# Kernel tuning notes

Measured on AMD Instinct MI355X. Metric: run time of the kernel, lower is better.

Reference implementation:

```python
import jax, jax.numpy as jnp
import numpy as np

N_HEAD = 16
N_KV = 4
HEAD_DIM = 128
WINDOW = 1024
SINK = 4
THETA = 10000.0


def _rope_cos_sin(T, dim, theta, dtype):
    inv_freq = 1.0 / (theta ** (jnp.arange(0, dim, 2, dtype=jnp.float32) / dim))
    t = jnp.arange(T, dtype=jnp.float32)
    ang = jnp.outer(t, inv_freq)  # [T, dim/2]
    return jnp.cos(ang).astype(dtype), jnp.sin(ang).astype(dtype)


def _apply_rope(x, cos, sin):
    # x: [B, H, T, D]; cos/sin: [T, D/2]
    d2 = x.shape[-1] // 2
    x1, x2 = x[..., :d2], x[..., d2:]
    return jnp.concatenate([x1 * cos - x2 * sin, x2 * cos + x1 * sin], axis=-1)


def setup_inputs() -> dict:
    key = jax.random.key(0)
    ks = jax.random.split(key, 5)
    B, T, C = 2, 2048, 2048
    x = jax.random.normal(ks[0], (B, T, C), dtype=jnp.float32)
    s = 0.02
    wq = jax.random.normal(ks[1], (C, C), dtype=jnp.float32) * s
    wk = jax.random.normal(ks[2], (N_KV * HEAD_DIM, C), dtype=jnp.float32) * s
    wv = jax.random.normal(ks[3], (N_KV * HEAD_DIM, C), dtype=jnp.float32) * s
    wo = jax.random.normal(ks[4], (C, C), dtype=jnp.float32) * s
    return {"x": x, "wq": wq, "wk": wk, "wv": wv, "wo": wo}


def reference(x, wq, wk, wv, wo):
    B, T, C = x.shape
    # QKV projections (Linear with weight [out, in], no bias)
    q = (x @ wq.T).reshape(B, T, N_HEAD, HEAD_DIM).transpose(0, 2, 1, 3)  # [B,H,T,D]
    k = (x @ wk.T).reshape(B, T, N_KV, HEAD_DIM).transpose(0, 2, 1, 3)    # [B,Hkv,T,D]
    v = (x @ wv.T).reshape(B, T, N_KV, HEAD_DIM).transpose(0, 2, 1, 3)

    cos, sin = _rope_cos_sin(T, HEAD_DIM, THETA, x.dtype)
    q = _apply_rope(q, cos, sin)
    k = _apply_rope(k, cos, sin)

    # GQA: repeat kv heads to match query heads (repeat_interleave on head dim)
    rep = N_HEAD // N_KV
    k = jnp.repeat(k, rep, axis=1)
    v = jnp.repeat(v, rep, axis=1)

    # causal + sliding window + attention sink mask
    i = jnp.arange(T)[:, None]
    j = jnp.arange(T)[None, :]
    allowed = (j <= i) & (((i - j) <= WINDOW) | (j < SINK))
    bias = jnp.where(allowed, 0.0, -jnp.inf).astype(x.dtype)  # [T,T]

    scale = 1.0 / np.sqrt(HEAD_DIM)
    att = jnp.einsum("bhqd,bhkd->bhqk", q, k) * scale + bias
    att = jax.nn.softmax(att, axis=-1)
    y = jnp.einsum("bhqk,bhkd->bhqd", att, v)  # [B,H,T,D]
    y = y.transpose(0, 2, 1, 3).reshape(B, T, C)
    return y @ wo.T
```

## Files before the change

kernel.cpp:

```cpp
#include <hip/hip_runtime.h>
#include <hip/hip_bf16.h>

typedef __bf16 bf16x8 __attribute__((ext_vector_type(8)));
typedef __bf16 bf16x4 __attribute__((ext_vector_type(4)));
typedef float  f32x4  __attribute__((ext_vector_type(4)));
typedef unsigned int uint4v __attribute__((ext_vector_type(4)));

#define NB     2
#define TT     2048
#define CC     2048
#define NH     16
#define NKV    4
#define HD     128
#define WIN    1024
#define SINKN  4
#define QSCALE 0.08838834764831845f

__device__ __forceinline__ void lds_load16(const void* g, void* l) {
    __builtin_amdgcn_global_load_lds(
        (__attribute__((address_space(1))) void*)const_cast<void*>(g),
        (__attribute__((address_space(3))) void*)l, 16, 0, 0);
}

__device__ __forceinline__ unsigned pack2bf(float a, float b) {
    __bf16 x = (__bf16)a, y = (__bf16)b;
    unsigned short ux = __builtin_bit_cast(unsigned short, x);
    unsigned short uy = __builtin_bit_cast(unsigned short, y);
    return (unsigned)ux | ((unsigned)uy << 16);
}

__global__ void cvt_kernel(const float* __restrict__ in, __bf16* __restrict__ out, int n) {
    int idx = (blockIdx.x * blockDim.x + threadIdx.x) * 4;
    const int stride = gridDim.x * blockDim.x * 4;
    for (; idx < n; idx += stride) {
        const float4 v = *(const float4*)(in + idx);
        bf16x4 o;
        o[0] = (__bf16)v.x; o[1] = (__bf16)v.y; o[2] = (__bf16)v.z; o[3] = (__bf16)v.w;
        *(bf16x4*)(out + idx) = o;
    }
}

__global__ void cvt_w_kernel(const float* __restrict__ wq, const float* __restrict__ wk,
                             const float* __restrict__ wv, const float* __restrict__ wo,
                             __bf16* __restrict__ out) {
    int idx = (blockIdx.x * blockDim.x + threadIdx.x) * 4;
    const int stride = gridDim.x * blockDim.x * 4;
    for (; idx < 10485760; idx += stride) {
        const float* src; int off;
        if (idx < 4194304)      { src = wq; off = idx; }
        else if (idx < 5242880) { src = wk; off = idx - 4194304; }
        else if (idx < 6291456) { src = wv; off = idx - 5242880; }
        else                    { src = wo; off = idx - 6291456; }
        const float4 v = *(const float4*)(src + off);
        bf16x4 o;
        o[0] = (__bf16)v.x; o[1] = (__bf16)v.y; o[2] = (__bf16)v.z; o[3] = (__bf16)v.w;
        *(bf16x4*)(out + idx) = o;
    }
}

__global__ void rope_table_kernel(float* __restrict__ cosT, float* __restrict__ sinT) {
    const int i = blockIdx.x * blockDim.x + threadIdx.x;
    const int t = i >> 6, d = i & 63;
    const float inv_freq = 1.0f / powf(10000.0f, (float)d * (1.0f / 64.0f));
    const float ang = (float)t * inv_freq;
    cosT[i] = cosf(ang);
    sinT[i] = sinf(ang);
}

__global__ void rope_scatter_kernel(const __bf16* __restrict__ qkv,
                                    const float* __restrict__ cosT,
                                    const float* __restrict__ sinT,
                                    __bf16* __restrict__ Qo,
                                    __bf16* __restrict__ Ko) {
    const int job = blockIdx.x * 256 + threadIdx.x;
    int m, d8, base_off; __bf16* outp; float scale;
    if (job < 524288) {
        m = job >> 7;
        const int pj = job & 127;
        const int hh = pj >> 3; d8 = pj & 7;
        base_off = hh * 128;
        const int b = m >> 11, t = m & 2047;
        outp = Qo + ((size_t)(b * NH + hh) * TT + t) * HD + d8 * 8;
        scale = QSCALE;
    } else {
        const int j2 = job - 524288;
        m = j2 >> 5;
        const int pj = j2 & 31;
        const int g = pj >> 3; d8 = pj & 7;
        base_off = 2048 + g * 128;
        const int b = m >> 11, t = m & 2047;
        outp = Ko + ((size_t)(b * NKV + g) * TT + t) * HD + d8 * 8;
        scale = 1.0f;
    }
    const int t = m & 2047;
    const __bf16* row = qkv + (size_t)m * 3072 + base_off + d8 * 8;
    const bf16x8 x1 = *(const bf16x8*)row;
    const bf16x8 x2 = *(const bf16x8*)(row + 64);
    const float4 c0 = *(const float4*)(cosT + t * 64 + d8 * 8);
    const float4 c1 = *(const float4*)(cosT + t * 64 + d8 * 8 + 4);
    const float4 s0 = *(const float4*)(sinT + t * 64 + d8 * 8);
    const float4 s1 = *(const float4*)(sinT + t * 64 + d8 * 8 + 4);
    const float cs[8] = {c0.x, c0.y, c0.z, c0.w, c1.x, c1.y, c1.z, c1.w};
    const float sn[8] = {s0.x, s0.y, s0.z, s0.w, s1.x, s1.y, s1.z, s1.w};
    bf16x8 o1, o2;
#pragma unroll
    for (int e = 0; e < 8; ++e) {
        const float a = (float)x1[e], bb = (float)x2[e];
        o1[e] = (__bf16)((a * cs[e] - bb * sn[e]) * scale);
        o2[e] = (__bf16)((bb * cs[e] + a * sn[e]) * scale);
    }
    *(bf16x8*)outp = o1;
    *(bf16x8*)(outp + 64) = o2;
}

__global__ void v_transpose_kernel(const __bf16* __restrict__ qkv, __bf16* __restrict__ Vt) {
    __shared__ __bf16 tile[64][72];
    const int bkv = blockIdx.z;
    const int b = bkv >> 2, g = bkv & 3;
    const int t0 = blockIdx.x << 6, d0 = blockIdx.y << 6;
    const int r = threadIdx.x >> 2, cg = threadIdx.x & 3;
    const __bf16* src = qkv + (size_t)(b * TT + t0 + r) * 3072 + 2560 + g * 128 + d0 + cg * 16;
    *(bf16x8*)&tile[r][cg * 16]     = *(const bf16x8*)src;
    *(bf16x8*)&tile[r][cg * 16 + 8] = *(const bf16x8*)(src + 8);
    __syncthreads();
    __bf16* dst = Vt + ((size_t)bkv * HD + d0 + r) * TT + t0 + cg * 16;
    bf16x8 o0, o1;
#pragma unroll
    for (int c2 = 0; c2 < 8; ++c2) {
        o0[c2] = tile[cg * 16 + c2][r];
        o1[c2] = tile[cg * 16 + 8 + c2][r];
    }
    *(bf16x8*)dst = o0;
    *(bf16x8*)(dst + 8) = o1;
}

template <int OUT_BF16>
__global__ __launch_bounds__(512, 2) void gemm_bt8(const __bf16* __restrict__ A,
                                                   const __bf16* __restrict__ Bm,
                                                   void* __restrict__ C,
                                                   int M, int N, int K) {
    __shared__ __align__(16) __bf16 lA[2][256 * 64];
    __shared__ __align__(16) __bf16 lB[2][256 * 64];
    const int tid = threadIdx.x;
    const int lane = tid & 63;
    const int w = tid >> 6;
    const int wm = w >> 2, wn = w & 3;
    const int nbn = N >> 8;
    const int bm = blockIdx.x / nbn, bn = blockIdx.x % nbn;
    const int m0 = bm << 8, n0 = bn << 8;
    const int lr = lane & 15, lh = lane >> 4;
    const int NT = K >> 6;

    auto stageA = [&](int kt, int buf, int i) {
        const int d = i * 8192 + tid * 16;
        const int row = d >> 7;
        const int colb = (d & 127) ^ ((row & 7) << 4);
        lds_load16(A + (size_t)(m0 + row) * K + kt * 64 + (colb >> 1),
                   (char*)lA[buf] + i * 8192 + w * 1024);
    };
    auto stageB = [&](int kt, int buf, int i) {
        const int d = i * 8192 + tid * 16;
        const int row = d >> 7;
        const int colb = (d & 127) ^ ((row & 7) << 4);
        lds_load16(Bm + (size_t)(n0 + row) * K + kt * 64 + (colb >> 1),
                   (char*)lB[buf] + i * 8192 + w * 1024);
    };

    f32x4 acc[8][4] = {};

#pragma unroll
    for (int i = 0; i < 4; ++i) stageA(0, 0, i);
#pragma unroll
    for (int i = 0; i < 4; ++i) stageB(0, 0, i);
    asm volatile("s_waitcnt vmcnt(0)" ::: "memory");
    __syncthreads();

    for (int kt = 0; kt < NT; ++kt) {
        const int cur = kt & 1, nxt = cur ^ 1;
        const bool pf = (kt + 1 < NT);
        const char* bA = (const char*)lA[cur];
        const char* bB = (const char*)lB[cur];

        bf16x8 aF[4][2], b0[2][2], b1[2][2];
#pragma unroll
        for (int mf = 0; mf < 4; ++mf)
#pragma unroll
            for (int ks = 0; ks < 2; ++ks) {
                const int row = wm * 128 + mf * 16 + lr;
                const int cb = (ks * 64 + lh * 16) ^ ((row & 7) << 4);
                aF[mf][ks] = *(const bf16x8*)(bA + row * 128 + cb);
            }
#pragma unroll
        for (int nf = 0; nf < 2; ++nf)
#pragma unroll
            for (int ks = 0; ks < 2; ++ks) {
                const int row = wn * 64 + nf * 16 + lr;
                const int cb = (ks * 64 + lh * 16) ^ ((row & 7) << 4);
                b0[nf][ks] = *(const bf16x8*)(bB + row * 128 + cb);
            }
        if (pf) { stageA(kt + 1, nxt, 0); stageA(kt + 1, nxt, 1); stageA(kt + 1, nxt, 2); stageA(kt + 1, nxt, 3); }
        __builtin_amdgcn_s_setprio(1);
#pragma unroll
        for (int mf = 0; mf < 4; ++mf)
#pragma unroll
            for (int nf = 0; nf < 2; ++nf)
#pragma unroll
                for (int ks = 0; ks < 2; ++ks)
                    acc[mf][nf] = __builtin_amdgcn_mfma_f32_16x16x32_bf16(aF[mf][ks], b0[nf][ks], acc[mf][nf], 0, 0, 0);
        __builtin_amdgcn_s_setprio(0);

#pragma unroll
        for (int nf = 0; nf < 2; ++nf)
#pragma unroll
            for (int ks = 0; ks < 2; ++ks) {
                const int row = wn * 64 + 32 + nf * 16 + lr;
                const int cb = (ks * 64 + lh * 16) ^ ((row & 7) << 4);
                b1[nf][ks] = *(const bf16x8*)(bB + row * 128 + cb);
            }
        if (pf) { stageB(kt + 1, nxt, 0); stageB(kt + 1, nxt, 1); stageB(kt + 1, nxt, 2); stageB(kt + 1, nxt, 3); }
        __builtin_amdgcn_s_setprio(1);
#pragma unroll
        for (int mf = 0; mf < 4; ++mf)
#pragma unroll
            for (int nf = 0; nf < 2; ++nf)
#pragma unroll
                for (int ks = 0; ks < 2; ++ks)
                    acc[mf][nf + 2] = __builtin_amdgcn_mfma_f32_16x16x32_bf16(aF[mf][ks], b1[nf][ks], acc[mf][nf + 2], 0, 0, 0);
        __builtin_amdgcn_s_setprio(0);

#pragma unroll
        for (int mf = 0; mf < 4; ++mf)
#pragma unroll
            for (int ks = 0; ks < 2; ++ks) {
                const int row = wm * 128 + 64 + mf * 16 + lr;
                const int cb = (ks * 64 + lh * 16) ^ ((row & 7) << 4);
                aF[mf][ks] = *(const bf16x8*)(bA + row * 128 + cb);
            }
        __builtin_amdgcn_s_setprio(1);
#pragma unroll
        for (int mf = 0; mf < 4; ++mf)
#pragma unroll
            for (int nf = 0; nf < 2; ++nf)
#pragma unroll
                for (int ks = 0; ks < 2; ++ks)
                    acc[mf + 4][nf] = __builtin_amdgcn_mfma_f32_16x16x32_bf16(aF[mf][ks], b0[nf][ks], acc[mf + 4][nf], 0, 0, 0);
        __builtin_amdgcn_s_setprio(0);

        __builtin_amdgcn_s_setprio(1);
#pragma unroll
        for (int mf = 0; mf < 4; ++mf)
#pragma unroll
            for (int nf = 0; nf < 2; ++nf)
#pragma unroll
                for (int ks = 0; ks < 2; ++ks)
                    acc[mf + 4][nf + 2] = __builtin_amdgcn_mfma_f32_16x16x32_bf16(aF[mf][ks], b1[nf][ks], acc[mf + 4][nf + 2], 0, 0, 0);
        __builtin_amdgcn_s_setprio(0);

        asm volatile("s_waitcnt vmcnt(0)" ::: "memory");
        __syncthreads();
    }

#pragma unroll
    for (int mf = 0; mf < 8; ++mf)
#pragma unroll
        for (int nf = 0; nf < 4; ++nf)
#pragma unroll
            for (int r = 0; r < 4; ++r) {
                const size_t row = m0 + wm * 128 + mf * 16 + lh * 4 + r;
                const size_t col = n0 + wn * 64 + nf * 16 + lr;
                if (OUT_BF16) ((__bf16*)C)[row * N + col] = (__bf16)acc[mf][nf][r];
                else          ((float*)C)[row * N + col]  = acc[mf][nf][r];
            }
}

template <int OUT_BF16>
__global__ __launch_bounds__(256, 2) void gemm_bt(const __bf16* __restrict__ A,
                                                  const __bf16* __restrict__ Bm,
                                                  void* __restrict__ C,
                                                  int M, int N, int K) {
    __shared__ __align__(16) __bf16 lA[2][128 * 32];
    __shared__ __align__(16) __bf16 lB[2][128 * 32];
    const int tid = threadIdx.x;
    const int lane = tid & 63;
    const int w = tid >> 6;
    const int wr = w >> 1, wc = w & 1;
    const int nbn = N >> 7;
    const int bm = blockIdx.x / nbn, bn = blockIdx.x % nbn;
    const int m0 = bm << 7, n0 = bn << 7;
    const int lr = lane & 15, lk = (lane >> 4) << 3;
    f32x4 acc[4][4] = {};

    auto stage = [&](int k0, int buf) {
#pragma unroll
        for (int L = 0; L < 2; ++L) {
            const int o = L * 4096 + w * 1024 + lane * 16;
            const int row = o >> 6, col = (o & 63) >> 1;
            lds_load16(A + (size_t)(m0 + row) * K + k0 + col, (char*)lA[buf] + L * 4096 + w * 1024);
            lds_load16(Bm + (size_t)(n0 + row) * K + k0 + col, (char*)lB[buf] + L * 4096 + w * 1024);
        }
    };

    stage(0, 0);
    asm volatile("s_waitcnt vmcnt(0)" ::: "memory");
    __syncthreads();

    const int NT = K >> 5;
    for (int kt = 0; kt < NT; ++kt) {
        const int buf = kt & 1;
        if (kt + 1 < NT) stage((kt + 1) << 5, buf ^ 1);

        bf16x8 af[4], bfr[4];
#pragma unroll
        for (int t = 0; t < 4; ++t) {
            af[t]  = *(const bf16x8*)&lA[buf][(wr * 64 + t * 16 + lr) * 32 + lk];
            bfr[t] = *(const bf16x8*)&lB[buf][(wc * 64 + t * 16 + lr) * 32 + lk];
        }
#pragma unroll
        for (int mt = 0; mt < 4; ++mt)
#pragma unroll
            for (int nt = 0; nt < 4; ++nt)
                acc[mt][nt] = __builtin_amdgcn_mfma_f32_16x16x32_bf16(af[mt], bfr[nt], acc[mt][nt], 0, 0, 0);

        asm volatile("s_waitcnt vmcnt(0)" ::: "memory");
        __syncthreads();
    }

    const int r0 = (lane >> 4) * 4;
#pragma unroll
    for (int mt = 0; mt < 4; ++mt)
#pragma unroll
        for (int nt = 0; nt < 4; ++nt)
#pragma unroll
            for (int r = 0; r < 4; ++r) {
                const size_t row = m0 + wr * 64 + mt * 16 + r0 + r;
                const size_t col = n0 + wc * 64 + nt * 16 + lr;
                if (OUT_BF16) ((__bf16*)C)[row * N + col] = (__bf16)acc[mt][nt][r];
                else          ((float*)C)[row * N + col]  = acc[mt][nt][r];
            }
}

__global__ __launch_bounds__(512, 4) void attn_kernel(const __bf16* __restrict__ Q,
                                                      const __bf16* __restrict__ Kg,
                                                      const __bf16* __restrict__ Vt,
                                                      __bf16* __restrict__ Y) {
    const int qt2 = 63 - blockIdx.x;
    const int kv = blockIdx.y, b = blockIdx.z;
    const int q0 = qt2 << 5;
    const int tid = threadIdx.x, lane = tid & 63, w = tid >> 6;
    const int lr = lane & 15, lh = lane >> 4;
    const int hh = w >> 1;
    const int h  = kv * 4 + hh;
    const int wh = w & 1;

    __shared__ __align__(16) __bf16 lK[64 * 128];
    __shared__ __align__(16) __bf16 lV[128 * 64];

    bf16x8 qf[4];
    {
        const __bf16* Qb = Q + ((size_t)(b * NH + h) * TT + q0 + wh * 16) * HD;
#pragma unroll
        for (int kc = 0; kc < 4; ++kc)
            qf[kc] = *(const bf16x8*)(Qb + lr * HD + kc * 32 + lh * 8);
    }

    f32x4 acc[8] = {};
    float mrun = -1e30f, lrun = 0.f;
    const int iq = q0 + wh * 16 + lr;

    const __bf16* Kb = Kg + (size_t)(b * NKV + kv) * TT * HD;
    const __bf16* Vb = Vt + (size_t)(b * NKV + kv) * HD * TT;
    const int jend = qt2 >> 1;
    const int jsw  = (q0 > WIN) ? ((q0 - WIN) >> 6) : 0;

    for (int jb = 0; jb <= jend; ++jb) {
        if (jb > 0 && jb < jsw) continue;
        const int j0 = jb << 6;
        __syncthreads();
#pragma unroll
        for (int L = 0; L < 2; ++L) {
            const int o = L * 8192 + w * 1024 + lane * 16;
            {
                const int row = o >> 8;
                const int colb = (o & 255) ^ ((row & 7) << 4);
                lds_load16(Kb + (size_t)(j0 + row) * HD + (colb >> 1), (char*)lK + L * 8192 + w * 1024);
            }
            {
                const int row = o >> 7;
                const int colb = (o & 127) ^ ((row & 7) << 4);
                lds_load16(Vb + (size_t)row * TT + j0 + (colb >> 1), (char*)lV + L * 8192 + w * 1024);
            }
        }
        asm volatile("s_waitcnt vmcnt(0)" ::: "memory");
        __syncthreads();

        f32x4 s4[4];
#pragma unroll
        for (int nt = 0; nt < 4; ++nt) {
            f32x4 s = {0.f, 0.f, 0.f, 0.f};
#pragma unroll
            for (int kc = 0; kc < 4; ++kc) {
                const int row = nt * 16 + lr;
                const int colb = ((kc * 32 + lh * 8) << 1) ^ ((row & 7) << 4);
                const bf16x8 kf = *(const bf16x8*)((const char*)lK + row * 256 + colb);
                s = __builtin_amdgcn_mfma_f32_16x16x32_bf16(kf, qf[kc], s, 0, 0, 0);
            }
            s4[nt] = s;
        }

        const bool fullTile = (j0 + 63 <= q0) && (q0 + 31 - j0 <= WIN);
        if (!fullTile) {
#pragma unroll
            for (int nt = 0; nt < 4; ++nt)
#pragma unroll
                for (int r = 0; r < 4; ++r) {
                    const int j = j0 + nt * 16 + lh * 4 + r;
                    const bool ok = (j <= iq) && ((iq - j <= WIN) || (j < SINKN));
                    if (!ok) s4[nt][r] = -1e30f;
                }
        }

        float mx = s4[0][0];
#pragma unroll
        for (int nt = 0; nt < 4; ++nt)
#pragma unroll
            for (int r = 0; r < 4; ++r) mx = fmaxf(mx, s4[nt][r]);
        mx = fmaxf(mx, __shfl_xor(mx, 16, 64));
        mx = fmaxf(mx, __shfl_xor(mx, 32, 64));

        if (!__all(mx - mrun <= 8.0f)) {
            const float mnew = fmaxf(mrun, mx);
            const float corr = __expf(mrun - mnew);
            mrun = mnew;
            lrun *= corr;
#pragma unroll
            for (int r = 0; r < 4; ++r) {
                const float c = __shfl(corr, lh * 4 + r, 64);
#pragma unroll
                for (int dt = 0; dt < 8; ++dt) acc[dt][r] *= c;
            }
        }

        float rsum = 0.f;
#pragma unroll
        for (int nt = 0; nt < 4; ++nt)
#pragma unroll
            for (int r = 0; r < 4; ++r) {
                const float p = __expf(s4[nt][r] - mrun);
                s4[nt][r] = p;
                rsum += p;
            }
        rsum += __shfl_xor(rsum, 16, 64);
        rsum += __shfl_xor(rsum, 32, 64);
        lrun += rsum;

        unsigned pw[4][2];
#pragma unroll
        for (int nt = 0; nt < 4; ++nt) {
            pw[nt][0] = pack2bf(s4[nt][0], s4[nt][1]);
            pw[nt][1] = pack2bf(s4[nt][2], s4[nt][3]);
        }
        bf16x8 pa[2];
#pragma unroll
        for (int kc = 0; kc < 2; ++kc) {
            uint4v wv;
#pragma unroll
            for (int widx = 0; widx < 4; ++widx) {
                const int m = widx & 1;
                const int srcl = lr + 16 * ((2 * lh + (widx >> 1)) & 3);
                const int wA = __shfl((int)pw[2 * kc][m], srcl, 64);
                const int wB = __shfl((int)pw[2 * kc + 1][m], srcl, 64);
                wv[widx] = (unsigned)((lh & 2) ? wB : wA);
            }
            pa[kc] = __builtin_bit_cast(bf16x8, wv);
        }

#pragma unroll
        for (int dt = 0; dt < 8; ++dt) {
#pragma unroll
            for (int kc = 0; kc < 2; ++kc) {
                const int row = dt * 16 + lr;
                const int colb = ((kc * 32 + lh * 8) << 1) ^ ((row & 7) << 4);
                const bf16x8 vf = *(const bf16x8*)((const char*)lV + row * 128 + colb);
                acc[dt] = __builtin_amdgcn_mfma_f32_16x16x32_bf16(pa[kc], vf, acc[dt], 0, 0, 0);
            }
        }
    }

    const float inv = 1.f / lrun;
#pragma unroll
    for (int r = 0; r < 4; ++r) {
        const float invr = __shfl(inv, lh * 4 + r, 64);
        const int trow = q0 + wh * 16 + lh * 4 + r;
        __bf16* Yp = Y + ((size_t)b * TT + trow) * CC + h * HD;
#pragma unroll
        for (int dt = 0; dt < 8; ++dt)
            Yp[dt * 16 + lr] = (__bf16)(acc[dt][r] * invr);
    }
}

extern "C" void kernel_launch(void* const* d_in, const int* in_sizes, int n_in,
                              void* d_out, int out_size, void* d_ws, size_t ws_size,
                              hipStream_t stream) {
    const float* x  = (const float*)d_in[0];
    const float* wq = (const float*)d_in[1];
    const float* wk = (const float*)d_in[2];
    const float* wv = (const float*)d_in[3];
    const float* wo = (const float*)d_in[4];
    float* out = (float*)d_out;

    char* ws = (char*)d_ws;
    size_t off = 0;
    auto alloc = [&](size_t bytes) { char* p = ws + off; off += bytes; return p; };
    __bf16* xb   = (__bf16*)alloc(16777216);
    __bf16* Wall = (__bf16*)alloc(12582912);
    __bf16* wob  = (__bf16*)alloc(8388608);
    __bf16* qkv  = (__bf16*)alloc(25165824);
    __bf16* Qs   = (__bf16*)alloc(16777216);
    __bf16* Ks   = (__bf16*)alloc(4194304);
    __bf16* Vts  = (__bf16*)alloc(4194304);
    float*  cosT = (float*)alloc(524288);
    float*  sinT = (float*)alloc(524288);
    __bf16* Yb = xb;

    cvt_kernel<<<2048, 256, 0, stream>>>(x, xb, 4096 * 2048);
    cvt_w_kernel<<<2048, 256, 0, stream>>>(wq, wk, wv, wo, Wall);
    rope_table_kernel<<<512, 256, 0, stream>>>(cosT, sinT);

    gemm_bt8<1><<<dim3(16 * 12), 512, 0, stream>>>(xb, Wall, qkv, 4096, 3072, 2048);
    rope_scatter_kernel<<<2560, 256, 0, stream>>>(qkv, cosT, sinT, Qs, Ks);
    v_transpose_kernel<<<dim3(32, 2, 8), 256, 0, stream>>>(qkv, Vts);
    attn_kernel<<<dim3(64, 4, 2), 512, 0, stream>>>(Qs, Ks, Vts, Yb);
    gemm_bt<0><<<dim3(32 * 16), 256, 0, stream>>>(Yb, wob, out, 4096, 2048, 2048);
}
```

Baseline: 189.8 us.

## Double-buffer K/V tiles in LDS to overlap global loads with attention compute

The attention kernel now keeps two LDS buffers for K and V. It prefetches the next KV tile asynchronously while computing on the current one, waiting with a partial vmcnt before a raw s_barrier. The loop is recast over a compact index that skips tiles masked out by the sliding window, with the sink tile visited first. This is meant to hide global-load latency behind the MFMA work. In exchange LDS use doubles to 64KB per block, which may lower occupancy below the launch_bounds target of 4 blocks. The vmcnt(4) count also depends on each thread issuing exactly four loads per stage.

```diff
diff --git a/kernel.cpp b/kernel.cpp
--- a/kernel.cpp
+++ b/kernel.cpp
@@ -352,8 +352,8 @@
     const int h  = kv * 4 + hh;
     const int wh = w & 1;
 
-    __shared__ __align__(16) __bf16 lK[64 * 128];
-    __shared__ __align__(16) __bf16 lV[128 * 64];
+    __shared__ __align__(16) __bf16 lK[2][64 * 128];
+    __shared__ __align__(16) __bf16 lV[2][128 * 64];
 
     bf16x8 qf[4];
     {
@@ -371,27 +371,45 @@
     const __bf16* Vb = Vt + (size_t)(b * NKV + kv) * HD * TT;
     const int jend = qt2 >> 1;
     const int jsw  = (q0 > WIN) ? ((q0 - WIN) >> 6) : 0;
-
-    for (int jb = 0; jb <= jend; ++jb) {
-        if (jb > 0 && jb < jsw) continue;
-        const int j0 = jb << 6;
-        __syncthreads();
+    const int jswe = (jsw < 1) ? 1 : jsw;
+    const int nv   = (jend >= jswe) ? (jend - jswe + 2) : 1;
+
+    auto stage = [&](int jb, int buf) {
+        const int j0s = jb << 6;
 #pragma unroll
         for (int L = 0; L < 2; ++L) {
             const int o = L * 8192 + w * 1024 + lane * 16;
             {
                 const int row = o >> 8;
                 const int colb = (o & 255) ^ ((row & 7) << 4);
-                lds_load16(Kb + (size_t)(j0 + row) * HD + (colb >> 1), (char*)lK + L * 8192 + w * 1024);
+                lds_load16(Kb + (size_t)(j0s + row) * HD + (colb >> 1),
+                           (char*)lK[buf] + L * 8192 + w * 1024);
             }
             {
                 const int row = o >> 7;
                 const int colb = (o & 127) ^ ((row & 7) << 4);
-                lds_load16(Vb + (size_t)row * TT + j0 + (colb >> 1), (char*)lV + L * 8192 + w * 1024);
-            }
-        }
-        asm volatile("s_waitcnt vmcnt(0)" ::: "memory");
-        __syncthreads();
+                lds_load16(Vb + (size_t)row * TT + j0s + (colb >> 1),
+                           (char*)lV[buf] + L * 8192 + w * 1024);
+            }
+        }
+    };
+
+    stage(0, 0);
+
+    for (int idx = 0; idx < nv; ++idx) {
+        const int cur = idx & 1;
+        const bool pf = (idx + 1 < nv);
+        const int jb = (idx == 0) ? 0 : (jswe + idx - 1);
+        const int j0 = jb << 6;
+
+        if (pf) stage(jswe + idx, cur ^ 1);
+        if (pf) asm volatile("s_waitcnt vmcnt(4)" ::: "memory");
+        else    asm volatile("s_waitcnt vmcnt(0)" ::: "memory");
+        __builtin_amdgcn_s_barrier();
+        __builtin_amdgcn_sched_barrier(0);
+
+        const char* bK = (const char*)lK[cur];
+        const char* bV = (const char*)lV[cur];
 
         f32x4 s4[4];
 #pragma unroll
@@ -401,7 +419,7 @@
             for (int kc = 0; kc < 4; ++kc) {
                 const int row = nt * 16 + lr;
                 const int colb = ((kc * 32 + lh * 8) << 1) ^ ((row & 7) << 4);
-                const bf16x8 kf = *(const bf16x8*)((const char*)lK + row * 256 + colb);
+                const bf16x8 kf = *(const bf16x8*)(bK + row * 256 + colb);
                 s = __builtin_amdgcn_mfma_f32_16x16x32_bf16(kf, qf[kc], s, 0, 0, 0);
             }
             s4[nt] = s;
@@ -480,10 +498,12 @@
             for (int kc = 0; kc < 2; ++kc) {
                 const int row = dt * 16 + lr;
                 const int colb = ((kc * 32 + lh * 8) << 1) ^ ((row & 7) << 4);
-                const bf16x8 vf = *(const bf16x8*)((const char*)lV + row * 128 + colb);
+                const bf16x8 vf = *(const bf16x8*)(bV + row * 128 + colb);
                 acc[dt] = __builtin_amdgcn_mfma_f32_16x16x32_bf16(pa[kc], vf, acc[dt], 0, 0, 0);
             }
         }
+
+        if (pf) __builtin_amdgcn_s_barrier();
     }
 
     const float inv = 1.f / lrun;
```

New measurement: 187.4 us. About the same (-1.3%).
